# Optimization experiments

Measured on AMD Instinct MI355X. Metric: run time of the kernel, lower is better.

Reference implementation:

```python
import jax, jax.numpy as jnp
import numpy as np

D = 256
H = 8
DH = D // H
N_NODES = 2048
N_EDGES = 4096
NEG = -10000.0
LN_EPS = 1e-5


def _layernorm(x, g, b):
    mu = jnp.mean(x, axis=-1, keepdims=True)
    var = jnp.var(x, axis=-1, keepdims=True)
    return (x - mu) * jax.lax.rsqrt(var + LN_EPS) * g + b


def setup_inputs() -> dict:
    key = jax.random.key(0)
    ks = jax.random.split(key, 20)
    s = 0.05
    x = jax.random.normal(ks[0], (N_NODES, D), jnp.float32)
    edge_index = jax.random.randint(ks[1], (2, N_EDGES), 0, N_NODES)
    edge_attr = jax.random.normal(ks[2], (N_EDGES, D), jnp.float32)
    edge_masks = jax.random.bernoulli(ks[3], 0.95, (N_EDGES, N_EDGES))
    return {
        "x": x,
        "edge_index": edge_index,
        "edge_attr": edge_attr,
        "edge_masks": edge_masks,
        # message MLP: Linear(3d, d) -> LeakyReLU(0.2) -> Linear(d, d)
        "W1": jax.random.normal(ks[4], (D, 3 * D), jnp.float32) * s,
        "b1": jnp.zeros((D,), jnp.float32),
        "W2": jax.random.normal(ks[5], (D, D), jnp.float32) * s,
        "b2": jnp.zeros((D,), jnp.float32),
        # MultiheadAttention params
        "in_proj_w": jax.random.normal(ks[6], (3 * D, D), jnp.float32) * s,
        "in_proj_b": jnp.zeros((3 * D,), jnp.float32),
        "out_w": jax.random.normal(ks[7], (D, D), jnp.float32) * s,
        "out_b": jnp.zeros((D,), jnp.float32),
        # GraphConv root weight + bias
        "root": jax.random.normal(ks[8], (D, D), jnp.float32) * s,
        "bias_p": jnp.zeros((D,), jnp.float32),
        # LayerNorms + residual linear
        "ln1_g": jnp.ones((D,), jnp.float32),
        "ln1_b": jnp.zeros((D,), jnp.float32),
        "ln2_g": jnp.ones((D,), jnp.float32),
        "ln2_b": jnp.zeros((D,), jnp.float32),
        "lin_w": jax.random.normal(ks[9], (D, D), jnp.float32) * s,
        "lin_b": jnp.zeros((D,), jnp.float32),
    }


def reference(x, edge_index, edge_attr, edge_masks,
              W1, b1, W2, b2,
              in_proj_w, in_proj_b, out_w, out_b,
              root, bias_p, ln1_g, ln1_b, ln2_g, ln2_b, lin_w, lin_b):
    # --- message: gather endpoints, concat with edge features, MLP ---
    x_j = x[edge_index[0]]            # source [E, d]
    x_i = x[edge_index[1]]            # target [E, d]
    h = jnp.concatenate([x_i, x_j, edge_attr], axis=1)          # [E, 3d]
    h = jax.nn.leaky_relu(h @ W1.T + b1, negative_slope=0.2)
    h = h @ W2.T + b2                                            # [E, d]

    # --- MultiheadAttention over edges (L=E, batch=1), eval mode ---
    qkv = h @ in_proj_w.T + in_proj_b                            # [E, 3d]
    q, k, v = jnp.split(qkv, 3, axis=1)
    q = q.reshape(N_EDGES, H, DH).transpose(1, 0, 2)             # [H, E, dh]
    k = k.reshape(N_EDGES, H, DH).transpose(1, 0, 2)
    v = v.reshape(N_EDGES, H, DH).transpose(1, 0, 2)
    scores = jnp.einsum('hed,hfd->hef', q, k) / np.sqrt(DH)      # [H, E, E]
    add_mask = jnp.where(edge_masks, 0.0, NEG).astype(scores.dtype)
    attn = jax.nn.softmax(scores + add_mask[None], axis=-1)
    o = jnp.einsum('hef,hfd->hed', attn, v)                      # [H, E, dh]
    o = o.transpose(1, 0, 2).reshape(N_EDGES, D)
    msg = o @ out_w.T + out_b                                    # [E, d]

    # --- scatter-add aggregation to target nodes + update ---
    aggr = jax.ops.segment_sum(msg, edge_index[1], num_segments=N_NODES)
    out = aggr + x @ root + bias_p                               # [N, d]

    # --- graph_block: norm1 -> residual linear -> norm2 ---
    y = _layernorm(out, ln1_g, ln1_b)
    y = _layernorm(y + (y @ lin_w.T + lin_b), ln2_g, ln2_b)
    return y
```

## Files before the change

kernel.cpp:

```cpp
#include <hip/hip_runtime.h>
#include <hip/hip_bf16.h>
#include <cstdint>

#define D_   256
#define E_   4096
#define NN_  2048

typedef float f32x4_t __attribute__((ext_vector_type(4)));
typedef short bf16x8_t __attribute__((ext_vector_type(8)));
typedef short bf16x4_t __attribute__((ext_vector_type(4)));

__device__ inline short f2bf(float f) {
    union { float fv; unsigned u; } v; v.fv = f;
    unsigned r = v.u + 0x7fffu + ((v.u >> 16) & 1u);
    return (short)(r >> 16);
}

__device__ inline unsigned cvtpk_bf16(float lo, float hi) {
    unsigned r;
    asm("v_cvt_pk_bf16_f32 %0, %1, %2" : "=v"(r) : "v"(lo), "v"(hi));
    return r;
}

__device__ inline float hw_exp2(float x) {
    float r;
    asm("v_exp_f32 %0, %1" : "=v"(r) : "v"(x));
    return r;
}

template<int ACT, bool GATHER, bool SCATTER, bool HASADD, bool ABF16, int OUT>
__global__ __launch_bounds__(512)
void mgemm_k(const void* __restrict__ A, const float* __restrict__ Bm,
             const float* __restrict__ bias, const float* __restrict__ addsrc,
             void* __restrict__ C, short* __restrict__ vtb,
             int M, int N, int K,
             const int* __restrict__ ei0, const int* __restrict__ ei1,
             const float* __restrict__ x, const float* __restrict__ eattr,
             float qsc)
{
    __shared__ char lds[32768];
    const int tid = threadIdx.x;
    const int w = tid >> 6, l = tid & 63;
    const int g = l >> 4, ln = l & 15;
    const int wr = w >> 1, wc = w & 1;
    const int m0 = blockIdx.x * 64, n0 = blockIdx.y * 64;

    const int srow = tid >> 3;
    const int sck  = (tid & 7) * 8;
    const int sswz = (srow & 7) << 4;
    int gi1 = 0, gi0 = 0;
    if (GATHER) { gi1 = ei1[m0 + srow]; gi0 = ei0[m0 + srow]; }

    f32x4_t acc[2];
    acc[0] = f32x4_t{0.f,0.f,0.f,0.f};
    acc[1] = f32x4_t{0.f,0.f,0.f,0.f};

    const int nt = K >> 6;
    float4 ga[2], gb[2];
    bf16x8_t gab;

    auto loadG = [&](int kk) {
        const int cb = kk + sck;
        if (ABF16) {
            gab = *(const bf16x8_t*)((const short*)A + (size_t)(m0 + srow) * K + cb);
        } else {
            const float* src;
            if (GATHER) {
                if (cb < 256)      src = x + (size_t)gi1 * 256 + cb;
                else if (cb < 512) src = x + (size_t)gi0 * 256 + (cb - 256);
                else               src = eattr + (size_t)(m0 + srow) * 256 + (cb - 512);
            } else {
                src = (const float*)A + (size_t)(m0 + srow) * K + cb;
            }
            ga[0] = *(const float4*)src;
            ga[1] = *(const float4*)(src + 4);
        }
        const float* bsrc = Bm + (size_t)(n0 + srow) * K + cb;
        gb[0] = *(const float4*)bsrc;
        gb[1] = *(const float4*)(bsrc + 4);
    };
    auto writeS = [&](int buf) {
        const int off = (srow*128 + sck*2) ^ sswz;
        if (ABF16) {
            *(bf16x8_t*)(lds + buf*8192 + off) = gab;
        } else {
            uint4 pa;
            pa.x = cvtpk_bf16(ga[0].x, ga[0].y); pa.y = cvtpk_bf16(ga[0].z, ga[0].w);
            pa.z = cvtpk_bf16(ga[1].x, ga[1].y); pa.w = cvtpk_bf16(ga[1].z, ga[1].w);
            *(uint4*)(lds + buf*8192 + off) = pa;
        }
        uint4 pb;
        pb.x = cvtpk_bf16(gb[0].x, gb[0].y); pb.y = cvtpk_bf16(gb[0].z, gb[0].w);
        pb.z = cvtpk_bf16(gb[1].x, gb[1].y); pb.w = cvtpk_bf16(gb[1].z, gb[1].w);
        *(uint4*)(lds + 16384 + buf*8192 + off) = pb;
    };

    loadG(0);
    writeS(0);
    __syncthreads();
    int cur = 0;
    for (int t = 0; t < nt; ++t) {
        if (t + 1 < nt) loadG((t + 1) << 6);
        #pragma unroll
        for (int kc = 0; kc < 2; kc++) {
            const int arow = wr*16 + ln;
            const bf16x8_t af = *(const bf16x8_t*)(lds + cur*8192 +
                    ((arow*128 + kc*64 + g*16) ^ ((arow&7)<<4)));
            #pragma unroll
            for (int n = 0; n < 2; n++) {
                const int brow = wc*32 + n*16 + ln;
                const bf16x8_t bfr = *(const bf16x8_t*)(lds + 16384 + cur*8192 +
                         ((brow*128 + kc*64 + g*16) ^ ((brow&7)<<4)));
                acc[n] = __builtin_amdgcn_mfma_f32_16x16x32_bf16(af, bfr, acc[n], 0, 0, 0);
            }
        }
        if (t + 1 < nt) writeS(cur ^ 1);
        __syncthreads();
        cur ^= 1;
    }

    #pragma unroll
    for (int n = 0; n < 2; n++) {
        const int col = n0 + wc*32 + n*16 + ln;
        const float bv = bias[col];
        const int row0 = m0 + wr*16 + g*4;
        float pv[4];
        #pragma unroll
        for (int r = 0; r < 4; r++) {
            float v = acc[n][r] + bv;
            if (ACT == 1) v = v > 0.f ? v : 0.2f * v;
            if (HASADD) v += addsrc[(size_t)(row0 + r) * N + col];
            pv[r] = v;
        }
        if (SCATTER) {
            #pragma unroll
            for (int r = 0; r < 4; r++)
                atomicAdd(&((float*)C)[(size_t)ei1[row0 + r] * 256 + col], pv[r]);
        } else if (OUT == 0) {
            #pragma unroll
            for (int r = 0; r < 4; r++)
                ((float*)C)[(size_t)(row0 + r) * N + col] = pv[r];
        } else if (OUT == 1) {
            #pragma unroll
            for (int r = 0; r < 4; r++)
                ((short*)C)[(size_t)(row0 + r) * N + col] =
                    f2bf((col < 256) ? pv[r] * qsc : pv[r]);
        } else {
            if (col < 512) {
                #pragma unroll
                for (int r = 0; r < 4; r++)
                    ((short*)C)[(size_t)(row0 + r) * 768 + col] =
                        f2bf((col < 256) ? pv[r] * qsc : pv[r]);
            } else {
                const int hd = (col - 512) >> 5, d = (col - 512) & 31;
                bf16x4_t pk;
                #pragma unroll
                for (int r = 0; r < 4; r++) pk[r] = f2bf(pv[r]);
                *(bf16x4_t*)(vtb + (size_t)hd*131072 + (size_t)d*4096 + row0) = pk;
            }
        }
    }
}

__global__ __launch_bounds__(256)
void prep_k(const int* __restrict__ mraw, unsigned int* __restrict__ pm,
            const float* __restrict__ root, float* __restrict__ rootT,
            float* __restrict__ aggr)
{
    __shared__ float T[64][65];
    const int bid = blockIdx.x;
    if (bid < 2048) {
        const int t = bid * 256 + threadIdx.x;
        aggr[t] = 0.f;
        const int row = t >> 7, wb = t & 127;
        unsigned int bits = 0;
        const uint4* p = (const uint4*)(mraw + (size_t)row * 4096 + wb * 32);
        #pragma unroll
        for (int g = 0; g < 8; g++) {
            const uint4 v = p[g];
            if (v.x) bits |= 1u << (g*4+0);
            if (v.y) bits |= 1u << (g*4+1);
            if (v.z) bits |= 1u << (g*4+2);
            if (v.w) bits |= 1u << (g*4+3);
        }
        pm[t] = bits;
    } else {
        const int bt = bid - 2048;
        const int m0 = (bt >> 2) * 64, n0 = (bt & 3) * 64;
        const int r = threadIdx.x >> 6, c = threadIdx.x & 63;
        #pragma unroll
        for (int i = 0; i < 16; i++)
            T[r + i*4][c] = root[(size_t)(m0 + r + i*4) * 256 + n0 + c];
        __syncthreads();
        #pragma unroll
        for (int i = 0; i < 16; i++)
            rootT[(size_t)(n0 + r + i*4) * 256 + m0 + c] = T[c][r + i*4];
    }
}

__global__ __launch_bounds__(512, 4)
void attn_k(const short* __restrict__ qkvb, const short* __restrict__ vt,
            const unsigned int* __restrict__ pmask, float* __restrict__ o)
{
    __shared__ char lds[49152];
    const int tid = threadIdx.x;
    const int w2 = tid >> 6, l = tid & 63;
    const int g = l >> 4, ln = l & 15;
    const int gi = w2 >> 2, wq = w2 & 3;
    const int head = blockIdx.x >> 6;
    const int q0 = (blockIdx.x & 63) * 64;
    const int qa = q0 + wq * 16 + ln;

    const bf16x8_t qf = *(const bf16x8_t*)(qkvb + (size_t)qa*768 + head*32 + g*8);

    f32x4_t oT0 = {0.f,0.f,0.f,0.f};
    f32x4_t oT1 = {0.f,0.f,0.f,0.f};
    float lsum = 0.f;

    const int st = tid & 255;
    const int skey = st >> 2, sc = st & 3;
    const int sd = st >> 3, skc = st & 7;
    const short* kgp = qkvb + 256 + head*32 + sc*8;
    const short* vgp = vt + (size_t)head*131072 + (size_t)sd*4096 + skc*8;
    char* Kg = lds + gi*8192;
    char* Vg = lds + 16384 + gi*8192;
    char* Pw = lds + 32768 + w2*2048;
    const unsigned int* mrow = pmask + (size_t)qa*128;
    const int kswz = (skey & 7) << 4, vswz = (sd & 7) << 4;
    const int pswz = (ln & 7) << 4;

    uint2 mwc;
    {
        const int k0 = gi * 64;
        const bf16x8_t kv = *(const bf16x8_t*)(kgp + (size_t)(k0 + skey)*768);
        *(bf16x8_t*)(Kg + ((skey*64 + sc*16) ^ kswz)) = kv;
        const bf16x8_t vv = *(const bf16x8_t*)(vgp + k0);
        *(bf16x8_t*)(Vg + ((sd*128 + skc*16) ^ vswz)) = vv;
        mwc = *(const uint2*)(mrow + gi*2);
    }

    for (int i = 0; i < 32; ++i) {
        __syncthreads();
        const int cur = i & 1;
        const int tt = 2*i + gi;
        uint2 mwn;
        if (i < 31) {
            const int k0n = (tt + 2) * 64;
            const bf16x8_t kv = *(const bf16x8_t*)(kgp + (size_t)(k0n + skey)*768);
            *(bf16x8_t*)(Kg + (cur^1)*4096 + ((skey*64 + sc*16) ^ kswz)) = kv;
            const bf16x8_t vv = *(const bf16x8_t*)(vgp + k0n);
            *(bf16x8_t*)(Vg + (cur^1)*4096 + ((sd*128 + skc*16) ^ vswz)) = vv;
            mwn = *(const uint2*)(mrow + (tt + 2)*2);
        }
        char* Kb = Kg + cur*4096;
        char* Vb = Vg + cur*4096;

        f32x4_t s[4];
        __builtin_amdgcn_s_setprio(1);
        #pragma unroll
        for (int kt = 0; kt < 4; kt++) {
            const int key = kt*16 + ln;
            const bf16x8_t kf = *(const bf16x8_t*)(Kb + ((key*64 + g*16) ^ ((key & 7) << 4)));
            f32x4_t z = {0.f,0.f,0.f,0.f};
            s[kt] = __builtin_amdgcn_mfma_f32_16x16x32_bf16(kf, qf, z, 0, 0, 0);
        }
        __builtin_amdgcn_s_setprio(0);

        #pragma unroll
        for (int kt = 0; kt < 4; kt++) {
            const unsigned word = (kt < 2) ? mwc.x : mwc.y;
            float p[4];
            #pragma unroll
            for (int r = 0; r < 4; r++) {
                const float e = hw_exp2(s[kt][r] - 17.312340490667562f);
                p[r] = ((word >> ((kt & 1)*16 + g*4 + r)) & 1u) ? e : 0.f;
            }
            lsum += (p[0] + p[1]) + (p[2] + p[3]);
            uint2 pk;
            pk.x = cvtpk_bf16(p[0], p[1]);
            pk.y = cvtpk_bf16(p[2], p[3]);
            *(uint2*)(Pw + ((ln*128 + kt*32 + g*8) ^ pswz)) = pk;
        }

        __builtin_amdgcn_s_setprio(1);
        #pragma unroll
        for (int kh = 0; kh < 2; kh++) {
            const bf16x8_t pf = *(const bf16x8_t*)(Pw + ((ln*128 + kh*64 + g*16) ^ pswz));
            const bf16x8_t vf0 = *(const bf16x8_t*)(Vb + ((ln*128 + kh*64 + g*16) ^ pswz));
            const bf16x8_t vf1 = *(const bf16x8_t*)(Vb + (((16+ln)*128 + kh*64 + g*16) ^ pswz));
            oT0 = __builtin_amdgcn_mfma_f32_16x16x32_bf16(vf0, pf, oT0, 0, 0, 0);
            oT1 = __builtin_amdgcn_mfma_f32_16x16x32_bf16(vf1, pf, oT1, 0, 0, 0);
        }
        __builtin_amdgcn_s_setprio(0);
        mwc = mwn;
    }

    __syncthreads();
    *(f32x4_t*)(lds + w2*2048 + l*32)      = oT0;
    *(f32x4_t*)(lds + w2*2048 + l*32 + 16) = oT1;
    ((float*)(lds + 16384))[w2*64 + l] = lsum;
    __syncthreads();
    if (gi == 0) {
        const int pw = w2 + 4;
        const f32x4_t b0 = *(const f32x4_t*)(lds + pw*2048 + l*32);
        const f32x4_t b1 = *(const f32x4_t*)(lds + pw*2048 + l*32 + 16);
        const float lp = ((const float*)(lds + 16384))[pw*64 + l];
        oT0 += b0; oT1 += b1;
        lsum += lp;
        lsum += __shfl_xor(lsum, 16);
        lsum += __shfl_xor(lsum, 32);
        const float inv = 1.0f / fmaxf(lsum, 1e-37f);
        float* op = o + (size_t)qa * 256 + head*32;
        float4 v0 = {oT0[0]*inv, oT0[1]*inv, oT0[2]*inv, oT0[3]*inv};
        float4 v1 = {oT1[0]*inv, oT1[1]*inv, oT1[2]*inv, oT1[3]*inv};
        *(float4*)(op + g*4) = v0;
        *(float4*)(op + 16 + g*4) = v1;
    }
}

__global__ __launch_bounds__(256)
void ln_k(const float* __restrict__ in, const float* __restrict__ g,
          const float* __restrict__ b, float* __restrict__ out)
{
    const int n = blockIdx.x, t = threadIdx.x;
    const float v = in[(size_t)n * 256 + t];
    float s1 = v, s2 = v * v;
    #pragma unroll
    for (int off = 32; off > 0; off >>= 1) {
        s1 += __shfl_xor(s1, off);
        s2 += __shfl_xor(s2, off);
    }
    __shared__ float r1[4], r2[4];
    const int wv = t >> 6;
    if ((t & 63) == 0) { r1[wv] = s1; r2[wv] = s2; }
    __syncthreads();
    const float t1 = r1[0] + r1[1] + r1[2] + r1[3];
    const float t2 = r2[0] + r2[1] + r2[2] + r2[3];
    const float mu  = t1 * (1.0f / 256.0f);
    const float var = t2 * (1.0f / 256.0f) - mu * mu;
    const float rs  = rsqrtf(var + 1e-5f);
    out[(size_t)n * 256 + t] = (v - mu) * rs * g[t] + b[t];
}

extern "C" void kernel_launch(void* const* d_in, const int* in_sizes, int n_in,
                              void* d_out, int out_size, void* d_ws, size_t ws_size,
                              hipStream_t stream)
{
    const float* x     = (const float*)d_in[0];
    const int*   ei    = (const int*)  d_in[1];
    const float* eattr = (const float*)d_in[2];
    const int*   mask  = (const int*)  d_in[3];
    const float* W1   = (const float*)d_in[4];
    const float* b1   = (const float*)d_in[5];
    const float* W2   = (const float*)d_in[6];
    const float* b2   = (const float*)d_in[7];
    const float* ipw  = (const float*)d_in[8];
    const float* ipb  = (const float*)d_in[9];
    const float* ow   = (const float*)d_in[10];
    const float* ob   = (const float*)d_in[11];
    const float* root = (const float*)d_in[12];
    const float* bp   = (const float*)d_in[13];
    const float* ln1g = (const float*)d_in[14];
    const float* ln1b = (const float*)d_in[15];
    const float* ln2g = (const float*)d_in[16];
    const float* ln2b = (const float*)d_in[17];
    const float* linw = (const float*)d_in[18];
    const float* linb = (const float*)d_in[19];
    const int* ei0 = ei;
    const int* ei1 = ei + E_;

    float* ws = (float*)d_ws;
    short* h1b   = (short*)ws;
    short* hb    = (short*)(ws + 524288);
    float* o     = ws + 1048576;
    float* y1    = ws + 1048576;
    float* z     = ws + 1572864;
    short* qkvb  = (short*)(ws + 2097152);
    float* aggr  = ws + 3670016;
    float* outb  = ws + 4194304;
    unsigned int* pmask = (unsigned int*)(ws + 4718592);
    short* vt    = (short*)(ws + 5242896);
    float* rootT = ws + 5767184;

    dim3 blk(256);
    dim3 blk512(512);
    prep_k<<<dim3(2064), blk, 0, stream>>>(mask, pmask, root, rootT, aggr);

    mgemm_k<1,true,false,false,false,1><<<dim3(64,4), blk512, 0, stream>>>(
        nullptr, W1, b1, nullptr, h1b, nullptr, E_, 256, 768, ei0, ei1, x, eattr, 1.0f);
    mgemm_k<0,false,false,false,true,1><<<dim3(64,4), blk512, 0, stream>>>(
        h1b, W2, b2, nullptr, hb, nullptr, E_, 256, 256, nullptr, nullptr, nullptr, nullptr, 1.0f);
    mgemm_k<0,false,false,false,true,2><<<dim3(64,12), blk512, 0, stream>>>(
        hb, ipw, ipb, nullptr, qkvb, vt, E_, 768, 256, nullptr, nullptr, nullptr, nullptr,
        0.25503486f);
    attn_k<<<dim3(512), dim3(512), 0, stream>>>(qkvb, vt, pmask, o);
    mgemm_k<0,false,true,false,false,0><<<dim3(64,4), blk512, 0, stream>>>(
        o, ow, ob, nullptr, aggr, nullptr, E_, 256, 256, nullptr, ei1, nullptr, nullptr, 1.0f);
    mgemm_k<0,false,false,true,false,0><<<dim3(32,4), blk512, 0, stream>>>(
        x, rootT, bp, aggr, outb, nullptr, NN_, 256, 256, nullptr, nullptr, nullptr, nullptr, 1.0f);
    ln_k<<<dim3(2048), blk, 0, stream>>>(outb, ln1g, ln1b, y1);
    mgemm_k<0,false,false,true,false,0><<<dim3(32,4), blk512, 0, stream>>>(
        y1, linw, linb, y1, z, nullptr, NN_, 256, 256, nullptr, nullptr, nullptr, nullptr, 1.0f);
    ln_k<<<dim3(2048), blk, 0, stream>>>(z, ln2g, ln2b, (float*)d_out);
}
```

Measured before the change: 110.6 us.

## Use 32-row GEMM tiles for node GEMMs and compute softmax sum via MFMA

Templates the GEMM on the M tile size and launches the two node-level GEMMs (M=2048) with 32-row tiles, doubling their block count so more CUs are busy. In the attention kernel, the per-row softmax denominator is now accumulated by an extra MFMA against a ones vector instead of scalar adds plus cross-lane shuffles. This trades one extra MFMA per step for fewer VALU ops, and the sum now uses the bf16-rounded probabilities, which matches the numerator more consistently.

Result: no change. 109.2 us (-1.3%).

```diff
diff --git a/kernel.cpp b/kernel.cpp
--- a/kernel.cpp
+++ b/kernel.cpp
@@ -28,7 +28,7 @@
     return r;
 }
 
-template<int ACT, bool GATHER, bool SCATTER, bool HASADD, bool ABF16, int OUT>
+template<int BM, int ACT, bool GATHER, bool SCATTER, bool HASADD, bool ABF16, int OUT>
 __global__ __launch_bounds__(512)
 void mgemm_k(const void* __restrict__ A, const float* __restrict__ Bm,
              const float* __restrict__ bias, const float* __restrict__ addsrc,
@@ -38,22 +38,27 @@
              const float* __restrict__ x, const float* __restrict__ eattr,
              float qsc)
 {
-    __shared__ char lds[32768];
+    constexpr int ASZ  = BM * 128;
+    constexpr int BOFF = 2 * ASZ;
+    constexpr int NFR  = (BM == 64) ? 2 : 1;
+    __shared__ char lds[BOFF + 16384];
     const int tid = threadIdx.x;
     const int w = tid >> 6, l = tid & 63;
     const int g = l >> 4, ln = l & 15;
-    const int wr = w >> 1, wc = w & 1;
-    const int m0 = blockIdx.x * 64, n0 = blockIdx.y * 64;
+    const int wr = (BM == 64) ? (w >> 1) : (w >> 2);
+    const int wc = (BM == 64) ? (w & 1)  : (w & 3);
+    const int m0 = blockIdx.x * BM, n0 = blockIdx.y * 64;
 
     const int srow = tid >> 3;
     const int sck  = (tid & 7) * 8;
     const int sswz = (srow & 7) << 4;
+    const bool doA = (BM == 64) || (tid < 256);
     int gi1 = 0, gi0 = 0;
     if (GATHER) { gi1 = ei1[m0 + srow]; gi0 = ei0[m0 + srow]; }
 
-    f32x4_t acc[2];
-    acc[0] = f32x4_t{0.f,0.f,0.f,0.f};
-    acc[1] = f32x4_t{0.f,0.f,0.f,0.f};
+    f32x4_t acc[NFR];
+    #pragma unroll
+    for (int n = 0; n < NFR; n++) acc[n] = f32x4_t{0.f,0.f,0.f,0.f};
 
     const int nt = K >> 6;
     float4 ga[2], gb[2];
@@ -61,19 +66,21 @@
 
     auto loadG = [&](int kk) {
         const int cb = kk + sck;
-        if (ABF16) {
-            gab = *(const bf16x8_t*)((const short*)A + (size_t)(m0 + srow) * K + cb);
-        } else {
-            const float* src;
-            if (GATHER) {
-                if (cb < 256)      src = x + (size_t)gi1 * 256 + cb;
-                else if (cb < 512) src = x + (size_t)gi0 * 256 + (cb - 256);
-                else               src = eattr + (size_t)(m0 + srow) * 256 + (cb - 512);
+        if (doA) {
+            if (ABF16) {
+                gab = *(const bf16x8_t*)((const short*)A + (size_t)(m0 + srow) * K + cb);
             } else {
-                src = (const float*)A + (size_t)(m0 + srow) * K + cb;
+                const float* src;
+                if (GATHER) {
+                    if (cb < 256)      src = x + (size_t)gi1 * 256 + cb;
+                    else if (cb < 512) src = x + (size_t)gi0 * 256 + (cb - 256);
+                    else               src = eattr + (size_t)(m0 + srow) * 256 + (cb - 512);
+                } else {
+                    src = (const float*)A + (size_t)(m0 + srow) * K + cb;
+                }
+                ga[0] = *(const float4*)src;
+                ga[1] = *(const float4*)(src + 4);
             }
-            ga[0] = *(const float4*)src;
-            ga[1] = *(const float4*)(src + 4);
         }
         const float* bsrc = Bm + (size_t)(n0 + srow) * K + cb;
         gb[0] = *(const float4*)bsrc;
@@ -81,18 +88,20 @@
     };
     auto writeS = [&](int buf) {
         const int off = (srow*128 + sck*2) ^ sswz;
-        if (ABF16) {
-            *(bf16x8_t*)(lds + buf*8192 + off) = gab;
-        } else {
-            uint4 pa;
-            pa.x = cvtpk_bf16(ga[0].x, ga[0].y); pa.y = cvtpk_bf16(ga[0].z, ga[0].w);
-            pa.z = cvtpk_bf16(ga[1].x, ga[1].y); pa.w = cvtpk_bf16(ga[1].z, ga[1].w);
-            *(uint4*)(lds + buf*8192 + off) = pa;
+        if (doA) {
+            if (ABF16) {
+                *(bf16x8_t*)(lds + buf*ASZ + off) = gab;
+            } else {
+                uint4 pa;
+                pa.x = cvtpk_bf16(ga[0].x, ga[0].y); pa.y = cvtpk_bf16(ga[0].z, ga[0].w);
+                pa.z = cvtpk_bf16(ga[1].x, ga[1].y); pa.w = cvtpk_bf16(ga[1].z, ga[1].w);
+                *(uint4*)(lds + buf*ASZ + off) = pa;
+            }
         }
         uint4 pb;
         pb.x = cvtpk_bf16(gb[0].x, gb[0].y); pb.y = cvtpk_bf16(gb[0].z, gb[0].w);
         pb.z = cvtpk_bf16(gb[1].x, gb[1].y); pb.w = cvtpk_bf16(gb[1].z, gb[1].w);
-        *(uint4*)(lds + 16384 + buf*8192 + off) = pb;
+        *(uint4*)(lds + BOFF + buf*8192 + off) = pb;
     };
 
     loadG(0);
@@ -104,12 +113,12 @@
         #pragma unroll
         for (int kc = 0; kc < 2; kc++) {
             const int arow = wr*16 + ln;
-            const bf16x8_t af = *(const bf16x8_t*)(lds + cur*8192 +
+            const bf16x8_t af = *(const bf16x8_t*)(lds + cur*ASZ +
                     ((arow*128 + kc*64 + g*16) ^ ((arow&7)<<4)));
             #pragma unroll
-            for (int n = 0; n < 2; n++) {
-                const int brow = wc*32 + n*16 + ln;
-                const bf16x8_t bfr = *(const bf16x8_t*)(lds + 16384 + cur*8192 +
+            for (int n = 0; n < NFR; n++) {
+                const int brow = (BM == 64 ? wc*32 + n*16 : wc*16) + ln;
+                const bf16x8_t bfr = *(const bf16x8_t*)(lds + BOFF + cur*8192 +
                          ((brow*128 + kc*64 + g*16) ^ ((brow&7)<<4)));
                 acc[n] = __builtin_amdgcn_mfma_f32_16x16x32_bf16(af, bfr, acc[n], 0, 0, 0);
             }
@@ -120,8 +129,8 @@
     }
 
     #pragma unroll
-    for (int n = 0; n < 2; n++) {
-        const int col = n0 + wc*32 + n*16 + ln;
+    for (int n = 0; n < NFR; n++) {
+        const int col = n0 + (BM == 64 ? wc*32 + n*16 : wc*16) + ln;
         const float bv = bias[col];
         const int row0 = m0 + wr*16 + g*4;
         float pv[4];
@@ -212,10 +221,13 @@
     const int qa = q0 + wq * 16 + ln;
 
     const bf16x8_t qf = *(const bf16x8_t*)(qkvb + (size_t)qa*768 + head*32 + g*8);
+    bf16x8_t ones;
+    #pragma unroll
+    for (int j = 0; j < 8; j++) ones[j] = (short)0x3F80;
 
     f32x4_t oT0 = {0.f,0.f,0.f,0.f};
     f32x4_t oT1 = {0.f,0.f,0.f,0.f};
-    float lsum = 0.f;
+    f32x4_t oS  = {0.f,0.f,0.f,0.f};
 
     const int st = tid & 255;
     const int skey = st >> 2, sc = st & 3;
@@ -275,7 +287,6 @@
                 const float e = hw_exp2(s[kt][r] - 17.312340490667562f);
                 p[r] = ((word >> ((kt & 1)*16 + g*4 + r)) & 1u) ? e : 0.f;
             }
-            lsum += (p[0] + p[1]) + (p[2] + p[3]);
             uint2 pk;
             pk.x = cvtpk_bf16(p[0], p[1]);
             pk.y = cvtpk_bf16(p[2], p[3]);
@@ -290,11 +301,13 @@
             const bf16x8_t vf1 = *(const bf16x8_t*)(Vb + (((16+ln)*128 + kh*64 + g*16) ^ pswz));
             oT0 = __builtin_amdgcn_mfma_f32_16x16x32_bf16(vf0, pf, oT0, 0, 0, 0);
             oT1 = __builtin_amdgcn_mfma_f32_16x16x32_bf16(vf1, pf, oT1, 0, 0, 0);
+            oS  = __builtin_amdgcn_mfma_f32_16x16x32_bf16(ones, pf, oS, 0, 0, 0);
         }
         __builtin_amdgcn_s_setprio(0);
         mwc = mwn;
     }
 
+    float lsum = oS[0];
     __syncthreads();
     *(f32x4_t*)(lds + w2*2048 + l*32)      = oT0;
     *(f32x4_t*)(lds + w2*2048 + l*32 + 16) = oT1;
@@ -307,8 +320,6 @@
         const float lp = ((const float*)(lds + 16384))[pw*64 + l];
         oT0 += b0; oT1 += b1;
         lsum += lp;
-        lsum += __shfl_xor(lsum, 16);
-        lsum += __shfl_xor(lsum, 32);
         const float inv = 1.0f / fmaxf(lsum, 1e-37f);
         float* op = o + (size_t)qa * 256 + head*32;
         float4 v0 = {oT0[0]*inv, oT0[1]*inv, oT0[2]*inv, oT0[3]*inv};
@@ -386,20 +397,20 @@
     dim3 blk512(512);
     prep_k<<<dim3(2064), blk, 0, stream>>>(mask, pmask, root, rootT, aggr);
 
-    mgemm_k<1,true,false,false,false,1><<<dim3(64,4), blk512, 0, stream>>>(
+    mgemm_k<64,1,true,false,false,false,1><<<dim3(64,4), blk512, 0, stream>>>(
         nullptr, W1, b1, nullptr, h1b, nullptr, E_, 256, 768, ei0, ei1, x, eattr, 1.0f);
-    mgemm_k<0,false,false,false,true,1><<<dim3(64,4), blk512, 0, stream>>>(
+    mgemm_k<64,0,false,false,false,true,1><<<dim3(64,4), blk512, 0, stream>>>(
         h1b, W2, b2, nullptr, hb, nullptr, E_, 256, 256, nullptr, nullptr, nullptr, nullptr, 1.0f);
-    mgemm_k<0,false,false,false,true,2><<<dim3(64,12), blk512, 0, stream>>>(
+    mgemm_k<64,0,false,false,false,true,2><<<dim3(64,12), blk512, 0, stream>>>(
         hb, ipw, ipb, nullptr, qkvb, vt, E_, 768, 256, nullptr, nullptr, nullptr, nullptr,
         0.25503486f);
     attn_k<<<dim3(512), dim3(512), 0, stream>>>(qkvb, vt, pmask, o);
-    mgemm_k<0,false,true,false,false,0><<<dim3(64,4), blk512, 0, stream>>>(
+    mgemm_k<64,0,false,true,false,false,0><<<dim3(64,4), blk512, 0, stream>>>(
         o, ow, ob, nullptr, aggr, nullptr, E_, 256, 256, nullptr, ei1, nullptr, nullptr, 1.0f);
-    mgemm_k<0,false,false,true,false,0><<<dim3(32,4), blk512, 0, stream>>>(
+    mgemm_k<32,0,false,false,true,false,0><<<dim3(64,4), blk512, 0, stream>>>(
         x, rootT, bp, aggr, outb, nullptr, NN_, 256, 256, nullptr, nullptr, nullptr, nullptr, 1.0f);
     ln_k<<<dim3(2048), blk, 0, stream>>>(outb, ln1g, ln1b, y1);
-    mgemm_k<0,false,false,true,false,0><<<dim3(32,4), blk512, 0, stream>>>(
+    mgemm_k<32,0,false,false,true,false,0><<<dim3(64,4), blk512, 0, stream>>>(
         y1, linw, linb, y1, z, nullptr, NN_, 256, 256, nullptr, nullptr, nullptr, nullptr, 1.0f);
     ln_k<<<dim3(2048), blk, 0, stream>>>(z, ln2g, ln2b, (float*)d_out);
 }
```
